# Performance work log

Hardware: AMD Instinct MI355X
Metric: run time of the kernel (lower is better)

## Reference

```python
import jax, jax.numpy as jnp
import numpy as np

D_MODEL = 1024
N_HEAD = 16


def setup_inputs() -> dict:
    key = jax.random.key(0)
    ks = jax.random.split(key, 11)
    B, T, D = 4, 2048, D_MODEL
    s = 1.0 / np.sqrt(D)
    inp = {
        "q": jax.random.normal(ks[0], (B, T, D), jnp.float32),
        "k": jax.random.normal(ks[1], (B, T, D), jnp.float32),
        "v": jax.random.normal(ks[2], (B, T, D), jnp.float32),
        "wq": jax.random.normal(ks[3], (D, D), jnp.float32) * s,
        "bq": jnp.zeros((D,), jnp.float32),
        "wk": jax.random.normal(ks[4], (D, D), jnp.float32) * s,
        "bk": jnp.zeros((D,), jnp.float32),
        "wv": jax.random.normal(ks[5], (D, D), jnp.float32) * s,
        "bv": jnp.zeros((D,), jnp.float32),
        "wo": jax.random.normal(ks[6], (D, D), jnp.float32) * s,
        "bo": jnp.zeros((D,), jnp.float32),
    }
    return inp


def reference(q, k, v, wq, bq, wk, bk, wv, bv, wo, bo):
    B, T, D = q.shape
    H = N_HEAD
    hd = D // H  # head dim
    # torch nn.Linear: y = x @ W.T + b
    qh = (q @ wq.T + bq).reshape(B, T, H, hd).transpose(0, 2, 1, 3)  # [B,H,T,hd]
    kh = (k @ wk.T + bk).reshape(B, T, H, hd).transpose(0, 2, 1, 3)
    vh = (v @ wv.T + bv).reshape(B, T, H, hd).transpose(0, 2, 1, 3)
    scale = 1.0 / jnp.sqrt(jnp.asarray(hd, qh.dtype))
    score = jnp.einsum("bhqd,bhkd->bhqk", qh, kh) * scale  # [B,H,T,T]
    causal = jnp.tril(jnp.ones((T, T), dtype=bool))
    score = jnp.where(causal, score, jnp.asarray(-jnp.inf, score.dtype))
    attn = jax.nn.softmax(score, axis=-1)
    out = jnp.einsum("bhqk,bhkd->bhqd", attn, vh)  # [B,H,T,hd]
    out = out.transpose(0, 2, 1, 3).reshape(B, T, D)
    return out @ wo.T + bo
```

## Files before the change

kernel.cpp:

```cpp
#include <hip/hip_runtime.h>
#include <hip/hip_bf16.h>

#define D_MODEL 1024
#define N_HEAD  16
#define HD      64
#define T_SEQ   2048
#define B_SZ    4
#define M_ROWS  (B_SZ * T_SEQ)

typedef __bf16 bf16;
typedef __bf16 bf16x4 __attribute__((ext_vector_type(4)));
typedef __bf16 bf16x8 __attribute__((ext_vector_type(8)));
typedef float  floatx4 __attribute__((ext_vector_type(4)));

__device__ __forceinline__ floatx4 fzero4() {
    floatx4 z = {0.f, 0.f, 0.f, 0.f};
    return z;
}

__device__ __forceinline__ bf16x8 cvt8(const float4 a, const float4 b) {
    bf16x8 o;
    o[0] = (bf16)a.x; o[1] = (bf16)a.y; o[2] = (bf16)a.z; o[3] = (bf16)a.w;
    o[4] = (bf16)b.x; o[5] = (bf16)b.y; o[6] = (bf16)b.z; o[7] = (bf16)b.w;
    return o;
}

__device__ __forceinline__ void async_ld16(const void* g, void* l) {
    __builtin_amdgcn_global_load_lds(
        (const __attribute__((address_space(1))) void*)g,
        (__attribute__((address_space(3))) void*)l,
        16, 0, 0);
}

struct CvtWArgs {
    const float* s[4];
    bf16* d[4];
};
__global__ __launch_bounds__(256) void cvtw_kernel(CvtWArgs a)
{
    const float* src = a.s[blockIdx.y];
    bf16* dst = a.d[blockIdx.y];
    const int n8 = D_MODEL * D_MODEL / 8;
    int i = blockIdx.x * blockDim.x + threadIdx.x;
    int stride = gridDim.x * blockDim.x;
    for (; i < n8; i += stride) {
        float4 x = ((const float4*)src)[2 * i];
        float4 y = ((const float4*)src)[2 * i + 1];
        ((bf16x8*)dst)[i] = cvt8(x, y);
    }
}

struct GemmArgs {
    const void* A[3];
    const bf16* W[3];
    const float* bias[3];
    void*       Out[3];
    float       scl[3];
    int         omode[3];
};

template <int AF32>
__global__ __launch_bounds__(256, 3) void gemm_k(GemmArgs g)
{
    __shared__ bf16 ldsA[128 * 64];
    __shared__ bf16 ldsW[2][128 * 64];

    const int z = blockIdx.z;
    const bf16* W     = g.W[z];
    const float* bias = g.bias[z];
    void* Out         = g.Out[z];
    const float scl   = g.scl[z];
    const int omode   = g.omode[z];

    const int tid  = threadIdx.x;
    const int wave = tid >> 6, lane = tid & 63;
    const int quad = lane >> 4, l15 = lane & 15;
    const int wr = wave >> 1, wc = wave & 1;
    const int m0 = blockIdx.x * 128, n0 = blockIdx.y * 128;

    floatx4 acc[4][4];
#pragma unroll
    for (int i = 0; i < 4; ++i)
#pragma unroll
        for (int j = 0; j < 4; ++j) acc[i][j] = fzero4();

    const int ro = lane >> 3;
    const int c8 = lane & 7;

    bf16* dA = &ldsA[(wave * 32 + ro) * 64 + (c8 ^ ro) * 8];
    const float* gAf = nullptr;
    const bf16*  gAb = nullptr;
    if constexpr (AF32)
        gAf = (const float*)g.A[z] + (size_t)(m0 + wave * 32 + ro) * 1024 + c8 * 8;
    else
        gAb = (const bf16*)g.A[z] + (size_t)(m0 + wave * 32 + ro) * 1024 + c8 * 8;

    const bf16* gW = W + (size_t)(n0 + wave * 32 + ro) * 1024 + (c8 ^ ro) * 8;

    float4 raf[4][2];
    bf16x8 rab[4];

#pragma unroll
    for (int j = 0; j < 4; ++j)
        async_ld16((const void*)(gW + (size_t)j * 8192), &ldsW[0][(wave * 32 + j * 8) * 64]);
#pragma unroll
    for (int j = 0; j < 4; ++j) {
        if constexpr (AF32) {
            raf[j][0] = *(const float4*)(gAf + (size_t)j * 8192);
            raf[j][1] = *(const float4*)(gAf + (size_t)j * 8192 + 4);
        } else {
            rab[j] = *(const bf16x8*)(gAb + (size_t)j * 8192);
        }
    }

    for (int kt = 0; kt < 16; ++kt) {
        const int cur = kt & 1;
        __syncthreads();
#pragma unroll
        for (int j = 0; j < 4; ++j) {
            if constexpr (AF32)
                *(bf16x8*)(dA + j * 8 * 64) = cvt8(raf[j][0], raf[j][1]);
            else
                *(bf16x8*)(dA + j * 8 * 64) = rab[j];
        }
        __syncthreads();

        if (kt < 15) {
            const int off = (kt + 1) * 64;
#pragma unroll
            for (int j = 0; j < 4; ++j)
                async_ld16((const void*)(gW + off + (size_t)j * 8192),
                           &ldsW[cur ^ 1][(wave * 32 + j * 8) * 64]);
#pragma unroll
            for (int j = 0; j < 4; ++j) {
                if constexpr (AF32) {
                    raf[j][0] = *(const float4*)(gAf + off + (size_t)j * 8192);
                    raf[j][1] = *(const float4*)(gAf + off + (size_t)j * 8192 + 4);
                } else {
                    rab[j] = *(const bf16x8*)(gAb + off + (size_t)j * 8192);
                }
            }
        }

#pragma unroll
        for (int ks = 0; ks < 2; ++ks) {
            const int pos = ((ks * 4 + quad) ^ (l15 & 7)) * 8;
            bf16x8 af[4], bw[4];
#pragma unroll
            for (int i = 0; i < 4; ++i)
                af[i] = *(const bf16x8*)(&ldsA[(wr * 64 + i * 16 + l15) * 64 + pos]);
#pragma unroll
            for (int j = 0; j < 4; ++j)
                bw[j] = *(const bf16x8*)(&ldsW[cur][(wc * 64 + j * 16 + l15) * 64 + pos]);
#pragma unroll
            for (int i = 0; i < 4; ++i)
#pragma unroll
                for (int j = 0; j < 4; ++j)
                    acc[i][j] = __builtin_amdgcn_mfma_f32_16x16x32_bf16(af[i], bw[j], acc[i][j], 0, 0, 0);
        }
    }

#pragma unroll
    for (int i = 0; i < 4; ++i) {
#pragma unroll
        for (int j = 0; j < 4; ++j) {
#pragma unroll
            for (int r = 0; r < 4; ++r) {
                int m = m0 + wr * 64 + i * 16 + quad * 4 + r;
                int n = n0 + wc * 64 + j * 16 + l15;
                float val = (acc[i][j][r] + bias[n]) * scl;
                if (omode == 2) {
                    ((float*)Out)[(size_t)m * 1024 + n] = val;
                } else {
                    int b = m >> 11, t = m & 2047;
                    int h = n >> 6,  d = n & 63;
                    size_t addr;
                    if (omode == 0)
                        addr = ((size_t)(b * N_HEAD + h) * T_SEQ + t) * HD + d;
                    else
                        addr = ((size_t)(b * N_HEAD + h) * HD + d) * T_SEQ + t;
                    ((bf16*)Out)[addr] = (bf16)val;
                }
            }
        }
    }
}

__global__ __launch_bounds__(256, 2) void attn_kernel(
    const bf16* __restrict__ Qh, const bf16* __restrict__ Kh,
    const bf16* __restrict__ Vt, bf16* __restrict__ AO)
{
    __shared__ bf16 Ks[128 * 64];
    __shared__ bf16 Vts[64 * 128];
    __shared__ bf16 Ps[128 * 72];

    const int tid  = threadIdx.x;
    const int wave = tid >> 6, lane = tid & 63;
    const int quad = lane >> 4, l15 = lane & 15;
    const int bh = blockIdx.y;
    const size_t base = (size_t)bh * T_SEQ * HD;
    const int bb = bh >> 4, hh = bh & 15;

    const int kro = lane >> 3;
    const int kgc = (lane & 7) ^ kro;
    const bf16* kgbase = Kh + base + (size_t)(wave * 32 + kro) * HD + kgc * 8;
    const int vrow_lo = lane >> 4;
    const int vchunk  = lane & 15;

    const bf16* vgbase[4];
    bf16* kdst[4];
    bf16* vdst[4];
#pragma unroll
    for (int j = 0; j < 4; ++j) {
        int d = wave * 16 + j * 4 + vrow_lo;
        int gcv = vchunk ^ (d & 15);
        vgbase[j] = Vt + base + (size_t)d * T_SEQ + gcv * 8;
        vdst[j]   = &Vts[d * 128 + vchunk * 8];
        kdst[j]   = &Ks[(wave * 32 + j * 8 + kro) * 64 + (lane & 7) * 8];
    }

    for (int phase = 0; phase < 2; ++phase) {
        const int qt = phase ? blockIdx.x : 15 - blockIdx.x;

        bf16x8 qf[2][2];
        const bf16* qbase = Qh + base + (size_t)(qt * 128 + wave * 32) * HD;
#pragma unroll
        for (int ti = 0; ti < 2; ++ti)
#pragma unroll
            for (int ks = 0; ks < 2; ++ks)
                qf[ti][ks] = *(const bf16x8*)(qbase + (ti * 16 + l15) * HD + ks * 32 + quad * 8);

        bf16x8 kreg[4], vreg[4];
#pragma unroll
        for (int j = 0; j < 4; ++j)
            kreg[j] = *(const bf16x8*)(kgbase + (size_t)(j * 8) * HD);
#pragma unroll
        for (int j = 0; j < 4; ++j)
            vreg[j] = *(const bf16x8*)(vgbase[j]);

        float mrow[2] = {-1e30f, -1e30f}, lrow[2] = {0.f, 0.f};
        floatx4 oacc[2][4];
#pragma unroll
        for (int ti = 0; ti < 2; ++ti)
#pragma unroll
            for (int nj = 0; nj < 4; ++nj) oacc[ti][nj] = fzero4();

        for (int kt = 0; kt <= qt; ++kt) {
            __syncthreads();
#pragma unroll
            for (int j = 0; j < 4; ++j) *(bf16x8*)kdst[j] = kreg[j];
#pragma unroll
            for (int j = 0; j < 4; ++j) *(bf16x8*)vdst[j] = vreg[j];
            __syncthreads();

            if (kt < qt) {
#pragma unroll
                for (int j = 0; j < 4; ++j)
                    kreg[j] = *(const bf16x8*)(kgbase + (size_t)((kt + 1) * 128 + j * 8) * HD);
#pragma unroll
                for (int j = 0; j < 4; ++j)
                    vreg[j] = *(const bf16x8*)(vgbase[j] + (kt + 1) * 128);
            }

            const bool diag = (kt == qt);
            const int lim = diag ? (2 * wave + 1) : 7;

            floatx4 sacc[2][8];
#pragma unroll
            for (int ti = 0; ti < 2; ++ti)
#pragma unroll
                for (int tj = 0; tj < 8; ++tj) sacc[ti][tj] = fzero4();
            __builtin_amdgcn_s_setprio(1);
#pragma unroll
            for (int ks = 0; ks < 2; ++ks) {
                const int pos = ((ks * 4 + quad) ^ (l15 & 7)) * 8;
#pragma unroll
                for (int tj = 0; tj < 8; ++tj) {
                    if (tj <= lim) {
                        bf16x8 kf = *(const bf16x8*)(&Ks[(tj * 16 + l15) * 64 + pos]);
                        sacc[0][tj] = __builtin_amdgcn_mfma_f32_16x16x32_bf16(kf, qf[0][ks], sacc[0][tj], 0, 0, 0);
                        sacc[1][tj] = __builtin_amdgcn_mfma_f32_16x16x32_bf16(kf, qf[1][ks], sacc[1][tj], 0, 0, 0);
                    }
                }
            }
            __builtin_amdgcn_s_setprio(0);

#pragma unroll
            for (int ti = 0; ti < 2; ++ti) {
                const int ql = wave * 32 + ti * 16 + l15;
                float mxp[4] = {-1e30f, -1e30f, -1e30f, -1e30f};
#pragma unroll
                for (int tj = 0; tj < 8; ++tj) {
                    if (tj <= lim) {
#pragma unroll
                        for (int r = 0; r < 4; ++r) {
                            float s = sacc[ti][tj][r];
                            if (diag && (tj * 16 + quad * 4 + r) > ql) s = -1e30f;
                            sacc[ti][tj][r] = s;
                            mxp[r] = fmaxf(mxp[r], s);
                        }
                    }
                }
                float mx = fmaxf(fmaxf(mxp[0], mxp[1]), fmaxf(mxp[2], mxp[3]));
                mx = fmaxf(mx, __shfl_xor(mx, 16));
                mx = fmaxf(mx, __shfl_xor(mx, 32));
                if (__any(mx > mrow[ti] + 8.0f)) {
                    float mnew  = fmaxf(mrow[ti], mx);
                    float alpha = exp2f(mrow[ti] - mnew);
                    mrow[ti] = mnew;
                    lrow[ti] *= alpha;
#pragma unroll
                    for (int r = 0; r < 4; ++r) {
                        float ar = __shfl(alpha, quad * 4 + r);
#pragma unroll
                        for (int nj = 0; nj < 4; ++nj)
                            oacc[ti][nj][r] *= ar;
                    }
                }
                float rs[4] = {0.f, 0.f, 0.f, 0.f};
#pragma unroll
                for (int tj = 0; tj < 8; ++tj) {
                    if (tj <= lim) {
#pragma unroll
                        for (int r = 0; r < 4; ++r) {
                            float p = exp2f(sacc[ti][tj][r] - mrow[ti]);
                            rs[r] += p;
                            sacc[ti][tj][r] = p;
                        }
                    }
                }
                float rsum = (rs[0] + rs[1]) + (rs[2] + rs[3]);
                rsum += __shfl_xor(rsum, 16);
                rsum += __shfl_xor(rsum, 32);
                lrow[ti] += rsum;
            }

#pragma unroll
            for (int h2 = 0; h2 < 2; ++h2) {
                if (4 * h2 > lim) break;
#pragma unroll
                for (int ti = 0; ti < 2; ++ti) {
                    const int ql = wave * 32 + ti * 16 + l15;
#pragma unroll
                    for (int tjo = 0; tjo < 4; ++tjo) {
                        int tj = 4 * h2 + tjo;
                        if (tj <= lim) {
                            bf16x4 pv;
#pragma unroll
                            for (int r = 0; r < 4; ++r) pv[r] = (bf16)sacc[ti][tj][r];
                            *(bf16x4*)(&Ps[ql * 72 + tjo * 16 + quad * 4]) = pv;
                        }
                    }
                }
#pragma unroll
                for (int ks2 = 0; ks2 < 2; ++ks2) {
                    const int gks = 2 * h2 + ks2;
                    if (diag && gks > wave) break;
                    bf16x8 pf[2];
                    pf[0] = *(const bf16x8*)(&Ps[(wave * 32 + l15) * 72 + ks2 * 32 + quad * 8]);
                    pf[1] = *(const bf16x8*)(&Ps[(wave * 32 + 16 + l15) * 72 + ks2 * 32 + quad * 8]);
                    __builtin_amdgcn_s_setprio(1);
#pragma unroll
                    for (int nj = 0; nj < 4; ++nj) {
                        int pos = ((gks * 4 + quad) ^ l15) * 8;
                        bf16x8 vf = *(const bf16x8*)(&Vts[(nj * 16 + l15) * 128 + pos]);
                        oacc[0][nj] = __builtin_amdgcn_mfma_f32_16x16x32_bf16(pf[0], vf, oacc[0][nj], 0, 0, 0);
                        oacc[1][nj] = __builtin_amdgcn_mfma_f32_16x16x32_bf16(pf[1], vf, oacc[1][nj], 0, 0, 0);
                    }
                    __builtin_amdgcn_s_setprio(0);
                }
            }
        }

#pragma unroll
        for (int ti = 0; ti < 2; ++ti) {
#pragma unroll
            for (int r = 0; r < 4; ++r) {
                float lv = __shfl(lrow[ti], quad * 4 + r);
                float rl = 1.f / lv;
                int qrow = qt * 128 + wave * 32 + ti * 16 + quad * 4 + r;
#pragma unroll
                for (int nj = 0; nj < 4; ++nj) {
                    int d = nj * 16 + l15;
                    AO[((size_t)(bb * T_SEQ + qrow)) * D_MODEL + hh * HD + d] =
                        (bf16)(oacc[ti][nj][r] * rl);
                }
            }
        }
    }
}

extern "C" void kernel_launch(void* const* d_in, const int* in_sizes, int n_in,
                              void* d_out, int out_size, void* d_ws, size_t ws_size,
                              hipStream_t stream)
{
    const float* q  = (const float*)d_in[0];
    const float* k  = (const float*)d_in[1];
    const float* v  = (const float*)d_in[2];
    const float* wq = (const float*)d_in[3];
    const float* bq = (const float*)d_in[4];
    const float* wk = (const float*)d_in[5];
    const float* bk = (const float*)d_in[6];
    const float* wv = (const float*)d_in[7];
    const float* bv = (const float*)d_in[8];
    const float* wo = (const float*)d_in[9];
    const float* bo = (const float*)d_in[10];

    char* ws  = (char*)d_ws;
    char* dob = (char*)d_out;
    const size_t MB = 1024 * 1024;

    bf16* Wqb = (bf16*)(ws);
    bf16* Wkb = (bf16*)(ws + 2 * MB);
    bf16* Wvb = (bf16*)(ws + 4 * MB);
    bf16* AO  = (bf16*)(ws + 6 * MB);
    bf16* Qh  = (bf16*)(ws + 22 * MB);
    bf16* Kh  = (bf16*)(ws + 38 * MB);
    bf16* Wob = (bf16*)(ws + 54 * MB);
    bf16* Vt  = (bf16*)(dob);

    const float QSCALE = 0.18033688011112042f;

    CvtWArgs cw;
    cw.s[0] = wq; cw.d[0] = Wqb;
    cw.s[1] = wk; cw.d[1] = Wkb;
    cw.s[2] = wv; cw.d[2] = Wvb;
    cw.s[3] = wo; cw.d[3] = Wob;

    GemmArgs gq;
    gq.A[0] = q; gq.W[0] = Wqb; gq.bias[0] = bq; gq.Out[0] = (void*)Qh; gq.scl[0] = QSCALE; gq.omode[0] = 0;
    gq.A[1] = k; gq.W[1] = Wkb; gq.bias[1] = bk; gq.Out[1] = (void*)Kh; gq.scl[1] = 1.0f;   gq.omode[1] = 0;
    gq.A[2] = v; gq.W[2] = Wvb; gq.bias[2] = bv; gq.Out[2] = (void*)Vt; gq.scl[2] = 1.0f;   gq.omode[2] = 1;

    GemmArgs go;
    go.A[0] = AO; go.W[0] = Wob; go.bias[0] = bo; go.Out[0] = d_out; go.scl[0] = 1.0f; go.omode[0] = 2;
    go.A[1] = AO; go.W[1] = Wob; go.bias[1] = bo; go.Out[1] = d_out; go.scl[1] = 1.0f; go.omode[1] = 2;
    go.A[2] = AO; go.W[2] = Wob; go.bias[2] = bo; go.Out[2] = d_out; go.scl[2] = 1.0f; go.omode[2] = 2;

    hipLaunchKernelGGL(cvtw_kernel, dim3(64, 4), dim3(256), 0, stream, cw);
    hipLaunchKernelGGL((gemm_k<1>), dim3(64, 8, 3), dim3(256), 0, stream, gq);
    hipLaunchKernelGGL(attn_kernel, dim3(8, 64), dim3(256), 0, stream, Qh, Kh, Vt, AO);
    hipLaunchKernelGGL((gemm_k<0>), dim3(64, 8, 1), dim3(256), 0, stream, go);
}
```

Measured before the change: 379.0 us.

## Double-buffer A register prefetch two tiles ahead with manual waitcnt scheduling

The projection GEMM now keeps two register sets for A tiles and issues global loads two k-steps ahead instead of one. It replaces __syncthreads with raw s_barrier, explicit vmcnt/lgkmcnt waits and sched_barrier fences, so only the older loads are waited on. The aim is to hide global load latency behind MFMA work. The cost is higher VGPR pressure, and the hand-counted vmcnt values must match the exact number of outstanding loads, including the async W loads.

```diff
diff --git a/kernel.cpp b/kernel.cpp
--- a/kernel.cpp
+++ b/kernel.cpp
@@ -97,51 +97,79 @@
 
     const bf16* gW = W + (size_t)(n0 + wave * 32 + ro) * 1024 + (c8 ^ ro) * 8;
 
-    float4 raf[4][2];
-    bf16x8 rab[4];
-
+    float4 raf0[4][2], raf1[4][2];
+    bf16x8 rab0[4],    rab1[4];
+
+#define LOAD_A_SET(RAF, RAB, OFF)                                              \
+    do {                                                                       \
+        if constexpr (AF32) {                                                  \
+            _Pragma("unroll")                                                  \
+            for (int j = 0; j < 4; ++j) {                                      \
+                RAF[j][0] = *(const float4*)(gAf + (OFF) + (size_t)j * 8192);  \
+                RAF[j][1] = *(const float4*)(gAf + (OFF) + (size_t)j * 8192 + 4);\
+            }                                                                  \
+        } else {                                                               \
+            _Pragma("unroll")                                                  \
+            for (int j = 0; j < 4; ++j)                                        \
+                RAB[j] = *(const bf16x8*)(gAb + (OFF) + (size_t)j * 8192);     \
+        }                                                                      \
+    } while (0)
+
+#define DSW_A_SET(RAF, RAB)                                                    \
+    do {                                                                       \
+        _Pragma("unroll")                                                      \
+        for (int j = 0; j < 4; ++j) {                                          \
+            if constexpr (AF32)                                                \
+                *(bf16x8*)(dA + j * 8 * 64) = cvt8(RAF[j][0], RAF[j][1]);      \
+            else                                                               \
+                *(bf16x8*)(dA + j * 8 * 64) = RAB[j];                          \
+        }                                                                      \
+    } while (0)
+
+    LOAD_A_SET(raf0, rab0, 0);
+    __builtin_amdgcn_sched_barrier(0);
 #pragma unroll
     for (int j = 0; j < 4; ++j)
         async_ld16((const void*)(gW + (size_t)j * 8192), &ldsW[0][(wave * 32 + j * 8) * 64]);
-#pragma unroll
-    for (int j = 0; j < 4; ++j) {
-        if constexpr (AF32) {
-            raf[j][0] = *(const float4*)(gAf + (size_t)j * 8192);
-            raf[j][1] = *(const float4*)(gAf + (size_t)j * 8192 + 4);
-        } else {
-            rab[j] = *(const bf16x8*)(gAb + (size_t)j * 8192);
-        }
-    }
+    __builtin_amdgcn_sched_barrier(0);
+    LOAD_A_SET(raf1, rab1, 64);
+    __builtin_amdgcn_sched_barrier(0);
 
     for (int kt = 0; kt < 16; ++kt) {
         const int cur = kt & 1;
-        __syncthreads();
-#pragma unroll
-        for (int j = 0; j < 4; ++j) {
-            if constexpr (AF32)
-                *(bf16x8*)(dA + j * 8 * 64) = cvt8(raf[j][0], raf[j][1]);
-            else
-                *(bf16x8*)(dA + j * 8 * 64) = rab[j];
-        }
-        __syncthreads();
-
+        __builtin_amdgcn_s_barrier();
         if (kt < 15) {
-            const int off = (kt + 1) * 64;
+            if constexpr (AF32) asm volatile("s_waitcnt vmcnt(8)" ::: "memory");
+            else                asm volatile("s_waitcnt vmcnt(4)" ::: "memory");
+        } else {
+            asm volatile("s_waitcnt vmcnt(0)" ::: "memory");
+        }
+        __builtin_amdgcn_sched_barrier(0);
+
+        if (cur == 0) DSW_A_SET(raf0, rab0);
+        else          DSW_A_SET(raf1, rab1);
+
+        if (kt < 15) {
+            const int woff = (kt + 1) * 64;
 #pragma unroll
             for (int j = 0; j < 4; ++j)
-                async_ld16((const void*)(gW + off + (size_t)j * 8192),
+                async_ld16((const void*)(gW + woff + (size_t)j * 8192),
                            &ldsW[cur ^ 1][(wave * 32 + j * 8) * 64]);
-#pragma unroll
-            for (int j = 0; j < 4; ++j) {
-                if constexpr (AF32) {
-                    raf[j][0] = *(const float4*)(gAf + off + (size_t)j * 8192);
-                    raf[j][1] = *(const float4*)(gAf + off + (size_t)j * 8192 + 4);
-                } else {
-                    rab[j] = *(const bf16x8*)(gAb + off + (size_t)j * 8192);
-                }
-            }
-        }
-
+        }
+        __builtin_amdgcn_sched_barrier(0);
+
+        if (kt < 14) {
+            const int aoff = (kt + 2) * 64;
+            if (cur == 0) LOAD_A_SET(raf0, rab0, aoff);
+            else          LOAD_A_SET(raf1, rab1, aoff);
+        }
+        __builtin_amdgcn_sched_barrier(0);
+
+        asm volatile("s_waitcnt lgkmcnt(0)" ::: "memory");
+        __builtin_amdgcn_s_barrier();
+        __builtin_amdgcn_sched_barrier(0);
+
+        const bf16* wcur = ldsW[cur];
 #pragma unroll
         for (int ks = 0; ks < 2; ++ks) {
             const int pos = ((ks * 4 + quad) ^ (l15 & 7)) * 8;
@@ -151,7 +179,7 @@
                 af[i] = *(const bf16x8*)(&ldsA[(wr * 64 + i * 16 + l15) * 64 + pos]);
 #pragma unroll
             for (int j = 0; j < 4; ++j)
-                bw[j] = *(const bf16x8*)(&ldsW[cur][(wc * 64 + j * 16 + l15) * 64 + pos]);
+                bw[j] = *(const bf16x8*)(&wcur[(wc * 64 + j * 16 + l15) * 64 + pos]);
 #pragma unroll
             for (int i = 0; i < 4; ++i)
 #pragma unroll
@@ -159,6 +187,8 @@
                     acc[i][j] = __builtin_amdgcn_mfma_f32_16x16x32_bf16(af[i], bw[j], acc[i][j], 0, 0, 0);
         }
     }
+#undef LOAD_A_SET
+#undef DSW_A_SET
 
 #pragma unroll
     for (int i = 0; i < 4; ++i) {
```

Result: slower. 393.9 us (+3.9%).
